# Kernel tuning notes

Measured on AMD Instinct MI355X. Metric: run time of the kernel, lower is better.

Reference implementation:

```python
import jax, jax.numpy as jnp
import numpy as np

HEADS = 16
D_MODEL = 1024
HEAD_DIM = D_MODEL // HEADS


def setup_inputs() -> dict:
    key = jax.random.key(0)
    ks = jax.random.split(key, 11)
    B, S, D = 2, 2048, D_MODEL
    s = 1.0 / np.sqrt(D)
    inp = {
        'Q': jax.random.normal(ks[0], (B, S, D), jnp.float32),
        'K': jax.random.normal(ks[1], (B, S, D), jnp.float32),
        'V': jax.random.normal(ks[2], (B, S, D), jnp.float32),
        'Wq': jax.random.normal(ks[3], (D, D), jnp.float32) * s,
        'Wk': jax.random.normal(ks[4], (D, D), jnp.float32) * s,
        'Wv': jax.random.normal(ks[5], (D, D), jnp.float32) * s,
        'Wo': jax.random.normal(ks[6], (D, D), jnp.float32) * s,
        'bq': jnp.zeros((D,), jnp.float32),
        'bk': jnp.zeros((D,), jnp.float32),
        'bv': jnp.zeros((D,), jnp.float32),
        'bo': jnp.zeros((D,), jnp.float32),
    }
    return inp


def reference(Q, K, V, Wq, Wk, Wv, Wo, bq, bk, bv, bo):
    B, S, D = Q.shape
    H, Dh = HEADS, HEAD_DIM
    # projections (torch Linear: x @ W.T + b)
    q = (Q @ Wq.T + bq).reshape(B, S, H, Dh).transpose(0, 2, 1, 3)  # [B,H,S,Dh]
    k = (K @ Wk.T + bk).reshape(B, S, H, Dh).transpose(0, 2, 1, 3)
    v = (V @ Wv.T + bv).reshape(B, S, H, Dh).transpose(0, 2, 1, 3)
    # naive scaled dot-product attention, scale = 1/sqrt(head_dim)
    scores = jnp.einsum('bhqd,bhkd->bhqk', q, k) / jnp.sqrt(jnp.float32(Dh))
    attn = jax.nn.softmax(scores, axis=-1)
    out = jnp.einsum('bhqk,bhkd->bhqd', attn, v)
    concat = out.transpose(0, 2, 1, 3).reshape(B, S, D)
    return concat @ Wo.T + bo
```

## Files before the change

kernel.cpp:

```cpp
#include <hip/hip_runtime.h>
#include <hip/hip_bf16.h>


#define SEQ     2048
#define DMODEL  1024
#define NHEADS  16
#define DH      64
#define MROWS   4096
#define M1      (1024*1024)
#define M4      (4*1024*1024)
#define SCQ     0.18033688f

typedef __hip_bfloat16 bf16;
typedef __attribute__((ext_vector_type(8))) short  short8;
typedef __attribute__((ext_vector_type(4))) float  f32x4;

__device__ __forceinline__ bf16 f2b(float x) { return __float2bfloat16(x); }
__device__ __forceinline__ f32x4 mfma16(short8 a, short8 b, f32x4 c) {
    return __builtin_amdgcn_mfma_f32_16x16x32_bf16(a, b, c, 0, 0, 0);
}
__device__ __forceinline__ unsigned pk2(float a, float b) {
    union { __hip_bfloat162 h; unsigned u; } x;
    x.h = __float22bfloat162_rn(float2{a, b});
    return x.u;
}
__device__ __forceinline__ short8 pk8(float4 a, float4 b) {
    union { short8 s; unsigned u[4]; } x;
    x.u[0] = pk2(a.x, a.y); x.u[1] = pk2(a.z, a.w);
    x.u[2] = pk2(b.x, b.y); x.u[3] = pk2(b.z, b.w);
    return x.s;
}
__device__ __forceinline__ float fexp2(float x) {
    return __builtin_amdgcn_exp2f(x);
}
#define GLDS(g, l) __builtin_amdgcn_global_load_lds( \
    (const __attribute__((address_space(1))) void*)(g), \
    (__attribute__((address_space(3))) void*)(l), 16, 0, 0)

__global__ __launch_bounds__(256) void cvt_all(
    const float* __restrict__ Wq, const float* __restrict__ Wk,
    const float* __restrict__ Wv, const float* __restrict__ Wo,
    const float* __restrict__ Q,  const float* __restrict__ K,
    const float* __restrict__ V,  bf16* __restrict__ dst)
{
    const size_t gid = (size_t)blockIdx.x * 256 + threadIdx.x;
    const size_t e0 = gid * 8;
    const float* s;
    if (e0 < (size_t)4 * M1) {
        const float* w[4] = {Wq, Wk, Wv, Wo};
        s = w[e0 >> 20] + (e0 & (M1 - 1));
    } else {
        const float* a[4] = {nullptr, Q, K, V};
        s = a[e0 >> 22] + (e0 & (M4 - 1));
    }
    float4 x = *(const float4*)s, y = *(const float4*)(s + 4);
    *(short8*)((short*)dst + e0) = pk8(x, y);
}

__global__ __launch_bounds__(256) void cvt_w(
    const float* __restrict__ W0, const float* __restrict__ W1,
    const float* __restrict__ W2, const float* __restrict__ W3,
    bf16* __restrict__ dst)
{
    const int gid = blockIdx.x * 256 + threadIdx.x;
    const int t   = gid >> 17;
    const int off = (gid & 131071) * 8;
    const float* srcs[4] = {W0, W1, W2, W3};
    const float* s = srcs[t] + off;
    float4 a = *(const float4*)s, b = *(const float4*)(s + 4);
    *(short8*)((short*)dst + (size_t)gid * 8) = pk8(a, b);
}

__global__ __launch_bounds__(256) void cvt_1(
    const float* __restrict__ X, bf16* __restrict__ D)
{
    const int gid = blockIdx.x * 256 + threadIdx.x;
    const int off = gid * 8;
    float4 a = *(const float4*)(X + off), b = *(const float4*)(X + off + 4);
    *(short8*)((short*)D + off) = pk8(a, b);
}

template <int BN>
__device__ __forceinline__ void gemm_body(
    const bf16* __restrict__ A, const bf16* __restrict__ B,
    const float* __restrict__ bias, void* __restrict__ outp,
    int m0, int n0, int mode, int bias_m, float scale)
{
    __shared__ short As[128 * 32];
    __shared__ short Bs[BN * 32];
    constexpr int NI = BN / 32;

    const int tid  = threadIdx.x;
    const int lane = tid & 63;
    const int wv   = tid >> 6;
    const int wm   = (wv >> 1) * 64;
    const int wn   = (wv & 1) * (BN / 2);
    const int fn   = lane & 15;
    const int fq   = lane >> 4;

    const int srow = lane >> 2;
    const int scol = (lane & 3) * 8;

    const short* Ag = (const short*)A;
    const short* Bg = (const short*)B;

    f32x4 acc[4][NI];
#pragma unroll
    for (int i = 0; i < 4; ++i)
#pragma unroll
        for (int j = 0; j < NI; ++j) acc[i][j] = (f32x4){0.f, 0.f, 0.f, 0.f};

    for (int k0 = 0; k0 < DMODEL; k0 += 32) {
#pragma unroll
        for (int i = 0; i < 2; ++i) {
            const int rr = wv * 32 + i * 16;
            const short* ga = Ag + (size_t)(m0 + rr + srow) * DMODEL + k0 + scol;
            GLDS(ga, As + rr * 32);
        }
#pragma unroll
        for (int i = 0; i < BN / 64; ++i) {
            const int rr = wv * (BN / 4) + i * 16;
            const short* gb = Bg + (size_t)(n0 + rr + srow) * DMODEL + k0 + scol;
            GLDS(gb, Bs + rr * 32);
        }
        __syncthreads();

        short8 af[4], bfr[NI];
#pragma unroll
        for (int im = 0; im < 4; ++im)
            af[im] = *(const short8*)(As + (wm + im * 16 + fn) * 32 + fq * 8);
#pragma unroll
        for (int in = 0; in < NI; ++in)
            bfr[in] = *(const short8*)(Bs + (wn + in * 16 + fn) * 32 + fq * 8);
#pragma unroll
        for (int im = 0; im < 4; ++im)
#pragma unroll
            for (int in = 0; in < NI; ++in)
                acc[im][in] = mfma16(af[im], bfr[in], acc[im][in]);
        __syncthreads();
    }

#pragma unroll
    for (int im = 0; im < 4; ++im) {
#pragma unroll
        for (int in = 0; in < NI; ++in) {
#pragma unroll
            for (int r = 0; r < 4; ++r) {
                const int m = m0 + wm + im * 16 + fq * 4 + r;
                const int n = n0 + wn + in * 16 + fn;
                const float c = (acc[im][in][r] + (bias_m ? bias[m] : bias[n])) * scale;
                if (mode == 0) {
                    ((float*)outp)[(size_t)m * DMODEL + n] = c;
                } else if (mode == 1) {
                    const int b = m >> 11, s = m & (SEQ - 1);
                    const int h = n >> 6,  d = n & (DH - 1);
                    ((bf16*)outp)[(((size_t)(b * NHEADS + h) * SEQ) + s) * DH + d] = f2b(c);
                } else {
                    const int h = m >> 6,  d = m & (DH - 1);
                    const int b = n >> 11, s = n & (SEQ - 1);
                    const int p = s & 31;
                    const int sp = (s & ~31) | ((p & 12) << 1) | ((p & 16) >> 2) | (p & 3);
                    ((bf16*)outp)[(((size_t)(b * NHEADS + h) * DH) + d) * SEQ + sp] = f2b(c);
                }
            }
        }
    }
}

__global__ __launch_bounds__(256, 3) void gemm_one(
    const bf16* A, const bf16* B, const float* bias, void* out,
    int mode, int bias_m, float scale)
{
    gemm_body<128>(A, B, bias, out, blockIdx.x * 128, blockIdx.y * 128,
                   mode, bias_m, scale);
}

__global__ __launch_bounds__(256, 3) void gemm_fin(
    const bf16* A, const bf16* B, const float* bias, void* out)
{
    gemm_body<64>(A, B, bias, out, blockIdx.x * 128, blockIdx.y * 64, 0, 0, 1.f);
}

__global__ __launch_bounds__(256, 3) void gemm_qkv(
    const bf16* Qb, const bf16* Kb, const bf16* Vb, const bf16* Wb,
    const float* bq, const float* bk, const float* bv,
    bf16* qp, bf16* kp, bf16* vp)
{
    const int blk = blockIdx.x;
    const int z = blk >> 8, t = blk & 255;
    if (z == 0)
        gemm_body<128>(Qb, Wb,          bq, qp, (t >> 3) * 128, (t & 7) * 128, 1, 0, SCQ);
    else if (z == 1)
        gemm_body<128>(Kb, Wb + M1,     bk, kp, (t >> 3) * 128, (t & 7) * 128, 1, 0, 1.f);
    else
        gemm_body<128>(Wb + 2 * M1, Vb, bv, vp, (t >> 5) * 128, (t & 31) * 128, 2, 1, 1.f);
}


#define QKG(KTB, G, S0, S1) { \
    const short* kr_ = (KTB) + ((G) * 16 + n) * 64; \
    short8 kf0_ = *(const short8*)(kr_ + off0); \
    short8 kf1_ = *(const short8*)(kr_ + off1); \
    S0 = mfma16(kf0_, qf00, Zv); S0 = mfma16(kf1_, qf01, S0); \
    S1 = mfma16(kf0_, qf10, Zv); S1 = mfma16(kf1_, qf11, S1); }

#define PKP(SA, SB, DST) { \
    union { short8 s8; unsigned u[4]; } bb_; \
    bb_.u[0] = pk2(fexp2(SA[0]), fexp2(SA[1])); \
    bb_.u[1] = pk2(fexp2(SA[2]), fexp2(SA[3])); \
    bb_.u[2] = pk2(fexp2(SB[0]), fexp2(SB[1])); \
    bb_.u[3] = pk2(fexp2(SB[2]), fexp2(SB[3])); \
    DST = bb_.s8; }

#define XPH(T, P00, P01, P10, P11) { \
    const short* KtB_ = Kb0 + ((T) & 1) * 4096; \
    f32x4 sa0_, sa1_, sb0_, sb1_; \
    QKG(KtB_, 0, sa0_, sa1_) \
    QKG(KtB_, 1, sb0_, sb1_) \
    PKP(sa0_, sb0_, P00) \
    PKP(sa1_, sb1_, P01) \
    QKG(KtB_, 2, sa0_, sa1_) \
    QKG(KtB_, 3, sb0_, sb1_) \
    PKP(sa0_, sb0_, P10) \
    PKP(sa1_, sb1_, P11) }

#define PVG(VTB, GD, P00, P01, P10, P11) { \
    const short* vr_ = (VTB) + ((GD) * 16 + n) * 64; \
    short8 vf0_ = *(const short8*)(vr_ + off0); \
    short8 vf1_ = *(const short8*)(vr_ + off1); \
    O[GD][0] = mfma16(vf0_, P00, O[GD][0]); \
    O[GD][0] = mfma16(vf1_, P10, O[GD][0]); \
    O[GD][1] = mfma16(vf0_, P01, O[GD][1]); \
    O[GD][1] = mfma16(vf1_, P11, O[GD][1]); }

#define YPH(T, P00, P01, P10, P11) { \
    const short* VtB_ = Vb0 + ((T) & 1) * 4096; \
    lc0 = mfma16(onesv, P00, lc0); \
    lc1 = mfma16(onesv, P01, lc1); \
    lc0 = mfma16(onesv, P10, lc0); \
    lc1 = mfma16(onesv, P11, lc1); \
    PVG(VtB_, 0, P00, P01, P10, P11) \
    PVG(VtB_, 1, P00, P01, P10, P11) \
    PVG(VtB_, 2, P00, P01, P10, P11) \
    PVG(VtB_, 3, P00, P01, P10, P11) }

__global__ __launch_bounds__(512, 4) void attn_fused(
    const bf16* __restrict__ q,
    const bf16* __restrict__ k,
    const bf16* __restrict__ vt,
    bf16* __restrict__ out)
{
    __shared__ short LB[32768];

    const int tid  = threadIdx.x;
    const int wave = tid >> 6;
    const int half = wave >> 2;
    const int w4   = wave & 3;
    const int lane = tid & 63;
    const int n    = lane & 15;
    const int quad = lane >> 4;

    const int blk  = blockIdx.x;
    const int xcd  = blk & 7;
    const int rest = blk >> 3;
    const int qt   = rest & 15;
    const int bh   = ((rest >> 4) << 3) | xcd;
    const int q0w  = qt * 128 + w4 * 32;
    const int kt0  = half * 16;

    const bf16* qhead = q  + (size_t)bh * SEQ * DH;
    const bf16* khead = k  + (size_t)bh * SEQ * DH;
    const bf16* vhead = vt + (size_t)bh * DH * SEQ;

    short* Kb0 = LB + half * 16384;
    short* Vb0 = LB + half * 16384 + 8192;

    short8 qf00, qf01, qf10, qf11;
    {
        const short* qr0 = (const short*)(qhead + (size_t)(q0w + n) * DH);
        qf00 = *(const short8*)(qr0 + quad * 8);
        qf01 = *(const short8*)(qr0 + 32 + quad * 8);
        const short* qr1 = (const short*)(qhead + (size_t)(q0w + 16 + n) * DH);
        qf10 = *(const short8*)(qr1 + quad * 8);
        qf11 = *(const short8*)(qr1 + 32 + quad * 8);
    }

    const short8 onesv = {(short)0x3F80, (short)0x3F80, (short)0x3F80, (short)0x3F80,
                          (short)0x3F80, (short)0x3F80, (short)0x3F80, (short)0x3F80};
    const f32x4 Zv = (f32x4){0.f, 0.f, 0.f, 0.f};

    f32x4 O[4][2];
#pragma unroll
    for (int gd = 0; gd < 4; ++gd)
#pragma unroll
        for (int qg = 0; qg < 2; ++qg) O[gd][qg] = Zv;
    f32x4 lc0 = Zv, lc1 = Zv;

    const int srow = lane >> 3;
    const int schk = (lane & 7) ^ srow;
    const int off0 = ((quad       ^ (n & 7)) * 8);
    const int off1 = (((4 + quad) ^ (n & 7)) * 8);

    auto stageK = [&](int kt, int buf) {
        const int kbase = kt * 64;
#pragma unroll
        for (int i = 0; i < 2; ++i) {
            const int r = w4 * 16 + i * 8 + srow;
            const char* gk = (const char*)(khead + (size_t)(kbase + r) * DH) + schk * 16;
            GLDS(gk, Kb0 + buf * 4096 + (w4 * 16 + i * 8) * 64);
        }
    };
    auto stageV = [&](int kt, int buf) {
        const int kbase = kt * 64;
#pragma unroll
        for (int i = 0; i < 2; ++i) {
            const int r = w4 * 16 + i * 8 + srow;
            const char* gv = (const char*)(vhead + (size_t)r * SEQ + kbase) + schk * 16;
            GLDS(gv, Vb0 + buf * 4096 + (w4 * 16 + i * 8) * 64);
        }
    };

    short8 PA00, PA01, PA10, PA11;
    short8 PB00, PB01, PB10, PB11;

    stageK(kt0, 0);

    __syncthreads();
    stageK(kt0 + 1, 1);
    stageV(kt0, 0);
    XPH(0, PA00, PA01, PA10, PA11)

#pragma unroll 1
    for (int t = 1; t < 15; t += 2) {
        __syncthreads();
        stageK(kt0 + t + 1, (t + 1) & 1);
        stageV(kt0 + t, t & 1);
        XPH(t, PB00, PB01, PB10, PB11)
        YPH(t - 1, PA00, PA01, PA10, PA11)
        __syncthreads();
        stageK(kt0 + t + 2, (t + 2) & 1);
        stageV(kt0 + t + 1, (t + 1) & 1);
        XPH(t + 1, PA00, PA01, PA10, PA11)
        YPH(t, PB00, PB01, PB10, PB11)
    }
    __syncthreads();
    stageV(kt0 + 15, 1);
    XPH(15, PB00, PB01, PB10, PB11)
    YPH(14, PA00, PA01, PA10, PA11)
    __syncthreads();
    YPH(15, PB00, PB01, PB10, PB11)

    float* scr = (float*)LB + (size_t)(w4 * 64 + lane) * 34;
    const float l0 = lc0[0];
    const float l1 = lc1[0];

    __syncthreads();
    if (half == 1) {
#pragma unroll
        for (int gd = 0; gd < 4; ++gd)
#pragma unroll
            for (int qg = 0; qg < 2; ++qg) {
                *(float2*)(scr + (gd * 2 + qg) * 4)     = float2{O[gd][qg][0], O[gd][qg][1]};
                *(float2*)(scr + (gd * 2 + qg) * 4 + 2) = float2{O[gd][qg][2], O[gd][qg][3]};
            }
        *(float2*)(scr + 32) = float2{l0, l1};
    }
    __syncthreads();
    if (half == 0) {
        const float2 lo = *(const float2*)(scr + 32);
        const float inv0 = 1.0f / (l0 + lo.x);
        const float inv1 = 1.0f / (l1 + lo.y);
        const int b = bh >> 4;
        const int h = bh & (NHEADS - 1);
#pragma unroll
        for (int gd = 0; gd < 4; ++gd) {
#pragma unroll
            for (int qg = 0; qg < 2; ++qg) {
                const float iv = qg ? inv1 : inv0;
                float2 a = *(const float2*)(scr + (gd * 2 + qg) * 4);
                float2 c = *(const float2*)(scr + (gd * 2 + qg) * 4 + 2);
                const int s = q0w + qg * 16 + n;
                uint2 o;
                o.x = pk2((O[gd][qg][0] + a.x) * iv, (O[gd][qg][1] + a.y) * iv);
                o.y = pk2((O[gd][qg][2] + c.x) * iv, (O[gd][qg][3] + c.y) * iv);
                *(uint2*)(out + ((size_t)(b * SEQ + s)) * DMODEL + h * DH + gd * 16 + quad * 4) = o;
            }
        }
    }
}

#undef QKG
#undef PKP
#undef XPH
#undef PVG
#undef YPH

__global__ __launch_bounds__(256) void attn_mfma(
    const bf16* __restrict__ q,
    const bf16* __restrict__ k,
    const bf16* __restrict__ vt,
    bf16* __restrict__ out)
{
    __shared__ short Kt[2][64 * 64];
    __shared__ short Vt[2][64 * 64];

    const int tid  = threadIdx.x;
    const int wave = tid >> 6;
    const int lane = tid & 63;
    const int n    = lane & 15;
    const int quad = lane >> 4;

    const int blk  = blockIdx.x;
    const int xcd  = blk & 7;
    const int rest = blk >> 3;
    const int qt   = rest & 15;
    const int bh   = ((rest >> 4) << 3) | xcd;
    const int q0w  = qt * 128 + wave * 32;

    const bf16* qhead = q  + (size_t)bh * SEQ * DH;
    const bf16* khead = k  + (size_t)bh * SEQ * DH;
    const bf16* vhead = vt + (size_t)bh * DH * SEQ;

    short8 qf[2][2];
#pragma unroll
    for (int qg = 0; qg < 2; ++qg) {
        const short* qr = (const short*)(qhead + (size_t)(q0w + qg * 16 + n) * DH);
        qf[qg][0] = *(const short8*)(qr + quad * 8);
        qf[qg][1] = *(const short8*)(qr + 32 + quad * 8);
    }

    const short8 onesv = {(short)0x3F80, (short)0x3F80, (short)0x3F80, (short)0x3F80,
                          (short)0x3F80, (short)0x3F80, (short)0x3F80, (short)0x3F80};
    const f32x4 Zv = (f32x4){0.f, 0.f, 0.f, 0.f};

    f32x4 O[4][2];
#pragma unroll
    for (int gd = 0; gd < 4; ++gd)
#pragma unroll
        for (int qg = 0; qg < 2; ++qg) O[gd][qg] = Zv;
    f32x4 lacc[2] = {Zv, Zv};

    const int srow = lane >> 3;
    const int schk = (lane & 7) ^ srow;
    const int off0 = ((quad       ^ (n & 7)) * 8);
    const int off1 = (((4 + quad) ^ (n & 7)) * 8);

    auto stage = [&](int kt, int buf) {
        const int kbase = kt * 64;
#pragma unroll
        for (int i = 0; i < 2; ++i) {
            const int r = wave * 16 + i * 8 + srow;
            const char* gk = (const char*)(khead + (size_t)(kbase + r) * DH) + schk * 16;
            const char* gv = (const char*)(vhead + (size_t)r * SEQ + kbase) + schk * 16;
            GLDS(gk, Kt[buf] + (wave * 16 + i * 8) * 64);
            GLDS(gv, Vt[buf] + (wave * 16 + i * 8) * 64);
        }
    };

    auto tile_body = [&](const short* KtB, const short* VtB) {
        f32x4 st[4][2];
#pragma unroll
        for (int g = 0; g < 4; ++g) {
            const short* kr = KtB + (g * 16 + n) * 64;
            short8 kf0 = *(const short8*)(kr + off0);
            short8 kf1 = *(const short8*)(kr + off1);
#pragma unroll
            for (int qg = 0; qg < 2; ++qg) {
                f32x4 s = mfma16(kf0, qf[qg][0], Zv);
                s = mfma16(kf1, qf[qg][1], s);
                st[g][qg] = s;
            }
        }
        short8 bP[2][2];
#pragma unroll
        for (int t = 0; t < 2; ++t) {
#pragma unroll
            for (int qg = 0; qg < 2; ++qg) {
                union { short8 s8; unsigned u[4]; } bb;
                bb.u[0] = pk2(fexp2(st[2*t][qg][0]),   fexp2(st[2*t][qg][1]));
                bb.u[1] = pk2(fexp2(st[2*t][qg][2]),   fexp2(st[2*t][qg][3]));
                bb.u[2] = pk2(fexp2(st[2*t+1][qg][0]), fexp2(st[2*t+1][qg][1]));
                bb.u[3] = pk2(fexp2(st[2*t+1][qg][2]), fexp2(st[2*t+1][qg][3]));
                bP[t][qg] = bb.s8;
                lacc[qg] = mfma16(onesv, bP[t][qg], lacc[qg]);
            }
        }
#pragma unroll
        for (int gd = 0; gd < 4; ++gd) {
            const short* vr = VtB + (gd * 16 + n) * 64;
            short8 vf0 = *(const short8*)(vr + off0);
            short8 vf1 = *(const short8*)(vr + off1);
#pragma unroll
            for (int qg = 0; qg < 2; ++qg) {
                O[gd][qg] = mfma16(vf0, bP[0][qg], O[gd][qg]);
                O[gd][qg] = mfma16(vf1, bP[1][qg], O[gd][qg]);
            }
        }
    };

    stage(0, 0);
#pragma unroll 1
    for (int kt = 0; kt < SEQ / 64; kt += 2) {
        __syncthreads();
        stage(kt + 1, 1);
        tile_body(Kt[0], Vt[0]);
        __syncthreads();
        if (kt + 2 < SEQ / 64) stage(kt + 2, 0);
        tile_body(Kt[1], Vt[1]);
    }

    const float inv0 = 1.0f / lacc[0][0];
    const float inv1 = 1.0f / lacc[1][0];
    const int b = bh >> 4;
    const int h = bh & (NHEADS - 1);
#pragma unroll
    for (int gd = 0; gd < 4; ++gd) {
#pragma unroll
        for (int qg = 0; qg < 2; ++qg) {
            const float iv = qg ? inv1 : inv0;
            const int s = q0w + qg * 16 + n;
            uint2 o;
            o.x = pk2(O[gd][qg][0] * iv, O[gd][qg][1] * iv);
            o.y = pk2(O[gd][qg][2] * iv, O[gd][qg][3] * iv);
            *(uint2*)(out + ((size_t)(b * SEQ + s)) * DMODEL + h * DH + gd * 16 + quad * 4) = o;
        }
    }
}

extern "C" void kernel_launch(void* const* d_in, const int* in_sizes, int n_in,
                              void* d_out, int out_size, void* d_ws, size_t ws_size,
                              hipStream_t stream) {
    const float* Q  = (const float*)d_in[0];
    const float* K  = (const float*)d_in[1];
    const float* V  = (const float*)d_in[2];
    const float* Wq = (const float*)d_in[3];
    const float* Wk = (const float*)d_in[4];
    const float* Wv = (const float*)d_in[5];
    const float* Wo = (const float*)d_in[6];
    const float* bq = (const float*)d_in[7];
    const float* bk = (const float*)d_in[8];
    const float* bv = (const float*)d_in[9];
    const float* bo = (const float*)d_in[10];

    bf16* kp = (bf16*)d_out;
    bf16* vp = kp + M4;

    dim3 bb(256);
    dim3 gqk(MROWS / 128, DMODEL / 128);
    dim3 gvv(DMODEL / 128, MROWS / 128);
    dim3 gfin(MROWS / 128, DMODEL / 64);

    if (ws_size >= (size_t)40 * 1024 * 1024) {
        bf16* Wb = (bf16*)d_ws;
        bf16* Qb = Wb + 4 * M1;
        bf16* Kb = Qb + M4;
        bf16* Vb = Kb + M4;
        bf16* qp = Vb + M4;
        bf16* ao = Qb;

        cvt_all<<<8192, bb, 0, stream>>>(Wq, Wk, Wv, Wo, Q, K, V, Wb);
        gemm_qkv<<<768, bb, 0, stream>>>(Qb, Kb, Vb, Wb, bq, bk, bv, qp, kp, vp);
        attn_fused<<<512, 512, 0, stream>>>(qp, kp, vp, ao);
        gemm_fin<<<gfin, bb, 0, stream>>>(ao, Wb + 3 * M1, bo, d_out);
    } else {
        bf16* Wb = (bf16*)d_ws;
        bf16* Xb = Wb + 4 * M1;
        bf16* qp = Xb + M4;
        bf16* ao = Xb;

        cvt_w<<<2048, bb, 0, stream>>>(Wq, Wk, Wv, Wo, Wb);
        cvt_1<<<2048, bb, 0, stream>>>(Q, Xb);
        gemm_one<<<gqk, bb, 0, stream>>>(Xb, Wb, bq, qp, 1, 0, SCQ);
        cvt_1<<<2048, bb, 0, stream>>>(K, Xb);
        gemm_one<<<gqk, bb, 0, stream>>>(Xb, Wb + M1, bk, kp, 1, 0, 1.f);
        cvt_1<<<2048, bb, 0, stream>>>(V, Xb);
        gemm_one<<<gvv, bb, 0, stream>>>(Wb + 2 * M1, Xb, bv, vp, 2, 1, 1.f);
        attn_mfma<<<512, bb, 0, stream>>>(qp, kp, vp, ao);
        gemm_fin<<<gfin, bb, 0, stream>>>(ao, Wb + 3 * M1, bo, d_out);
    }
}
```

Measured before the change: 209.9 us.

## Give each attention wave 64 query rows with 256-thread blocks

Blocks in the fused attention kernel drop from 8 waves to 4, so each wave now handles 64 query rows instead of 32. Every K and V fragment read from shared memory then feeds twice as many MFMAs, and staging is split across fewer waves with more loads each. The cost is roughly doubled accumulator and P registers per wave, plus fewer waves per block to hide latency.

```diff
diff --git a/kernel.cpp b/kernel.cpp
--- a/kernel.cpp
+++ b/kernel.cpp
@@ -197,54 +197,53 @@
 }
 
 
-#define QKG(KTB, G, S0, S1) { \
-    const short* kr_ = (KTB) + ((G) * 16 + n) * 64; \
-    short8 kf0_ = *(const short8*)(kr_ + off0); \
-    short8 kf1_ = *(const short8*)(kr_ + off1); \
-    S0 = mfma16(kf0_, qf00, Zv); S0 = mfma16(kf1_, qf01, S0); \
-    S1 = mfma16(kf0_, qf10, Zv); S1 = mfma16(kf1_, qf11, S1); }
-
-#define PKP(SA, SB, DST) { \
-    union { short8 s8; unsigned u[4]; } bb_; \
-    bb_.u[0] = pk2(fexp2(SA[0]), fexp2(SA[1])); \
-    bb_.u[1] = pk2(fexp2(SA[2]), fexp2(SA[3])); \
-    bb_.u[2] = pk2(fexp2(SB[0]), fexp2(SB[1])); \
-    bb_.u[3] = pk2(fexp2(SB[2]), fexp2(SB[3])); \
-    DST = bb_.s8; }
-
-#define XPH(T, P00, P01, P10, P11) { \
+#define XPH(T, P) { \
     const short* KtB_ = Kb0 + ((T) & 1) * 4096; \
-    f32x4 sa0_, sa1_, sb0_, sb1_; \
-    QKG(KtB_, 0, sa0_, sa1_) \
-    QKG(KtB_, 1, sb0_, sb1_) \
-    PKP(sa0_, sb0_, P00) \
-    PKP(sa1_, sb1_, P01) \
-    QKG(KtB_, 2, sa0_, sa1_) \
-    QKG(KtB_, 3, sb0_, sb1_) \
-    PKP(sa0_, sb0_, P10) \
-    PKP(sa1_, sb1_, P11) }
-
-#define PVG(VTB, GD, P00, P01, P10, P11) { \
-    const short* vr_ = (VTB) + ((GD) * 16 + n) * 64; \
-    short8 vf0_ = *(const short8*)(vr_ + off0); \
-    short8 vf1_ = *(const short8*)(vr_ + off1); \
-    O[GD][0] = mfma16(vf0_, P00, O[GD][0]); \
-    O[GD][0] = mfma16(vf1_, P10, O[GD][0]); \
-    O[GD][1] = mfma16(vf0_, P01, O[GD][1]); \
-    O[GD][1] = mfma16(vf1_, P11, O[GD][1]); }
-
-#define YPH(T, P00, P01, P10, P11) { \
+    _Pragma("unroll") \
+    for (int tt = 0; tt < 2; ++tt) { \
+        f32x4 st[2][4]; \
+        _Pragma("unroll") \
+        for (int g2 = 0; g2 < 2; ++g2) { \
+            const short* kr_ = KtB_ + ((tt * 2 + g2) * 16 + n) * 64; \
+            short8 kf0_ = *(const short8*)(kr_ + off0); \
+            short8 kf1_ = *(const short8*)(kr_ + off1); \
+            _Pragma("unroll") \
+            for (int qg = 0; qg < 4; ++qg) { \
+                f32x4 s_ = mfma16(kf0_, qf[qg][0], Zv); \
+                st[g2][qg] = mfma16(kf1_, qf[qg][1], s_); \
+            } \
+        } \
+        _Pragma("unroll") \
+        for (int qg = 0; qg < 4; ++qg) { \
+            union { short8 s8; unsigned u[4]; } bb_; \
+            bb_.u[0] = pk2(fexp2(st[0][qg][0]), fexp2(st[0][qg][1])); \
+            bb_.u[1] = pk2(fexp2(st[0][qg][2]), fexp2(st[0][qg][3])); \
+            bb_.u[2] = pk2(fexp2(st[1][qg][0]), fexp2(st[1][qg][1])); \
+            bb_.u[3] = pk2(fexp2(st[1][qg][2]), fexp2(st[1][qg][3])); \
+            P[tt][qg] = bb_.s8; \
+        } \
+    } }
+
+#define YPH(T, P) { \
     const short* VtB_ = Vb0 + ((T) & 1) * 4096; \
-    lc0 = mfma16(onesv, P00, lc0); \
-    lc1 = mfma16(onesv, P01, lc1); \
-    lc0 = mfma16(onesv, P10, lc0); \
-    lc1 = mfma16(onesv, P11, lc1); \
-    PVG(VtB_, 0, P00, P01, P10, P11) \
-    PVG(VtB_, 1, P00, P01, P10, P11) \
-    PVG(VtB_, 2, P00, P01, P10, P11) \
-    PVG(VtB_, 3, P00, P01, P10, P11) }
-
-__global__ __launch_bounds__(512, 4) void attn_fused(
+    _Pragma("unroll") \
+    for (int qg = 0; qg < 4; ++qg) { \
+        lc[qg] = mfma16(onesv, P[0][qg], lc[qg]); \
+        lc[qg] = mfma16(onesv, P[1][qg], lc[qg]); \
+    } \
+    _Pragma("unroll") \
+    for (int gd = 0; gd < 4; ++gd) { \
+        const short* vr_ = VtB_ + (gd * 16 + n) * 64; \
+        short8 vf0_ = *(const short8*)(vr_ + off0); \
+        short8 vf1_ = *(const short8*)(vr_ + off1); \
+        _Pragma("unroll") \
+        for (int qg = 0; qg < 4; ++qg) { \
+            O[gd][qg] = mfma16(vf0_, P[0][qg], O[gd][qg]); \
+            O[gd][qg] = mfma16(vf1_, P[1][qg], O[gd][qg]); \
+        } \
+    } }
+
+__global__ __launch_bounds__(256, 2) void attn_fused(
     const bf16* __restrict__ q,
     const bf16* __restrict__ k,
     const bf16* __restrict__ vt,
@@ -254,8 +253,8 @@
 
     const int tid  = threadIdx.x;
     const int wave = tid >> 6;
-    const int half = wave >> 2;
-    const int w4   = wave & 3;
+    const int half = wave >> 1;
+    const int wq   = wave & 1;
     const int lane = tid & 63;
     const int n    = lane & 15;
     const int quad = lane >> 4;
@@ -265,7 +264,7 @@
     const int rest = blk >> 3;
     const int qt   = rest & 15;
     const int bh   = ((rest >> 4) << 3) | xcd;
-    const int q0w  = qt * 128 + w4 * 32;
+    const int q0w  = qt * 128 + wq * 64;
     const int kt0  = half * 16;
 
     const bf16* qhead = q  + (size_t)bh * SEQ * DH;
@@ -275,26 +274,26 @@
     short* Kb0 = LB + half * 16384;
     short* Vb0 = LB + half * 16384 + 8192;
 
-    short8 qf00, qf01, qf10, qf11;
-    {
-        const short* qr0 = (const short*)(qhead + (size_t)(q0w + n) * DH);
-        qf00 = *(const short8*)(qr0 + quad * 8);
-        qf01 = *(const short8*)(qr0 + 32 + quad * 8);
-        const short* qr1 = (const short*)(qhead + (size_t)(q0w + 16 + n) * DH);
-        qf10 = *(const short8*)(qr1 + quad * 8);
-        qf11 = *(const short8*)(qr1 + 32 + quad * 8);
+    short8 qf[4][2];
+#pragma unroll
+    for (int qg = 0; qg < 4; ++qg) {
+        const short* qr = (const short*)(qhead + (size_t)(q0w + qg * 16 + n) * DH);
+        qf[qg][0] = *(const short8*)(qr + quad * 8);
+        qf[qg][1] = *(const short8*)(qr + 32 + quad * 8);
     }
 
     const short8 onesv = {(short)0x3F80, (short)0x3F80, (short)0x3F80, (short)0x3F80,
                           (short)0x3F80, (short)0x3F80, (short)0x3F80, (short)0x3F80};
     const f32x4 Zv = (f32x4){0.f, 0.f, 0.f, 0.f};
 
-    f32x4 O[4][2];
+    f32x4 O[4][4];
 #pragma unroll
     for (int gd = 0; gd < 4; ++gd)
 #pragma unroll
-        for (int qg = 0; qg < 2; ++qg) O[gd][qg] = Zv;
-    f32x4 lc0 = Zv, lc1 = Zv;
+        for (int qg = 0; qg < 4; ++qg) O[gd][qg] = Zv;
+    f32x4 lc[4];
+#pragma unroll
+    for (int qg = 0; qg < 4; ++qg) lc[qg] = Zv;
 
     const int srow = lane >> 3;
     const int schk = (lane & 7) ^ srow;
@@ -304,81 +303,81 @@
     auto stageK = [&](int kt, int buf) {
         const int kbase = kt * 64;
 #pragma unroll
-        for (int i = 0; i < 2; ++i) {
-            const int r = w4 * 16 + i * 8 + srow;
+        for (int i = 0; i < 4; ++i) {
+            const int r = wq * 32 + i * 8 + srow;
             const char* gk = (const char*)(khead + (size_t)(kbase + r) * DH) + schk * 16;
-            GLDS(gk, Kb0 + buf * 4096 + (w4 * 16 + i * 8) * 64);
+            GLDS(gk, Kb0 + buf * 4096 + (wq * 32 + i * 8) * 64);
         }
     };
     auto stageV = [&](int kt, int buf) {
         const int kbase = kt * 64;
 #pragma unroll
-        for (int i = 0; i < 2; ++i) {
-            const int r = w4 * 16 + i * 8 + srow;
+        for (int i = 0; i < 4; ++i) {
+            const int r = wq * 32 + i * 8 + srow;
             const char* gv = (const char*)(vhead + (size_t)r * SEQ + kbase) + schk * 16;
-            GLDS(gv, Vb0 + buf * 4096 + (w4 * 16 + i * 8) * 64);
+            GLDS(gv, Vb0 + buf * 4096 + (wq * 32 + i * 8) * 64);
         }
     };
 
-    short8 PA00, PA01, PA10, PA11;
-    short8 PB00, PB01, PB10, PB11;
+    short8 PA[2][4], PB[2][4];
 
     stageK(kt0, 0);
 
     __syncthreads();
     stageK(kt0 + 1, 1);
     stageV(kt0, 0);
-    XPH(0, PA00, PA01, PA10, PA11)
+    XPH(0, PA)
 
 #pragma unroll 1
     for (int t = 1; t < 15; t += 2) {
         __syncthreads();
         stageK(kt0 + t + 1, (t + 1) & 1);
         stageV(kt0 + t, t & 1);
-        XPH(t, PB00, PB01, PB10, PB11)
-        YPH(t - 1, PA00, PA01, PA10, PA11)
+        XPH(t, PB)
+        YPH(t - 1, PA)
         __syncthreads();
         stageK(kt0 + t + 2, (t + 2) & 1);
         stageV(kt0 + t + 1, (t + 1) & 1);
-        XPH(t + 1, PA00, PA01, PA10, PA11)
-        YPH(t, PB00, PB01, PB10, PB11)
+        XPH(t + 1, PA)
+        YPH(t, PB)
     }
     __syncthreads();
     stageV(kt0 + 15, 1);
-    XPH(15, PB00, PB01, PB10, PB11)
-    YPH(14, PA00, PA01, PA10, PA11)
+    XPH(15, PB)
+    YPH(14, PA)
     __syncthreads();
-    YPH(15, PB00, PB01, PB10, PB11)
-
-    float* scr = (float*)LB + (size_t)(w4 * 64 + lane) * 34;
-    const float l0 = lc0[0];
-    const float l1 = lc1[0];
+    YPH(15, PB)
+
+    float* scr = (float*)LB + (size_t)(wq * 64 + lane) * 68;
 
     __syncthreads();
     if (half == 1) {
 #pragma unroll
         for (int gd = 0; gd < 4; ++gd)
 #pragma unroll
-            for (int qg = 0; qg < 2; ++qg) {
-                *(float2*)(scr + (gd * 2 + qg) * 4)     = float2{O[gd][qg][0], O[gd][qg][1]};
-                *(float2*)(scr + (gd * 2 + qg) * 4 + 2) = float2{O[gd][qg][2], O[gd][qg][3]};
+            for (int qg = 0; qg < 4; ++qg) {
+                *(float2*)(scr + (gd * 4 + qg) * 4)     = float2{O[gd][qg][0], O[gd][qg][1]};
+                *(float2*)(scr + (gd * 4 + qg) * 4 + 2) = float2{O[gd][qg][2], O[gd][qg][3]};
             }
-        *(float2*)(scr + 32) = float2{l0, l1};
+        *(float4*)(scr + 64) = float4{lc[0][0], lc[1][0], lc[2][0], lc[3][0]};
     }
     __syncthreads();
     if (half == 0) {
-        const float2 lo = *(const float2*)(scr + 32);
-        const float inv0 = 1.0f / (l0 + lo.x);
-        const float inv1 = 1.0f / (l1 + lo.y);
+        const float4 lo = *(const float4*)(scr + 64);
+        float inv[4];
+        inv[0] = 1.0f / (lc[0][0] + lo.x);
+        inv[1] = 1.0f / (lc[1][0] + lo.y);
+        inv[2] = 1.0f / (lc[2][0] + lo.z);
+        inv[3] = 1.0f / (lc[3][0] + lo.w);
         const int b = bh >> 4;
         const int h = bh & (NHEADS - 1);
 #pragma unroll
         for (int gd = 0; gd < 4; ++gd) {
 #pragma unroll
-            for (int qg = 0; qg < 2; ++qg) {
-                const float iv = qg ? inv1 : inv0;
-                float2 a = *(const float2*)(scr + (gd * 2 + qg) * 4);
-                float2 c = *(const float2*)(scr + (gd * 2 + qg) * 4 + 2);
+            for (int qg = 0; qg < 4; ++qg) {
+                const float iv = inv[qg];
+                float2 a = *(const float2*)(scr + (gd * 4 + qg) * 4);
+                float2 c = *(const float2*)(scr + (gd * 4 + qg) * 4 + 2);
                 const int s = q0w + qg * 16 + n;
                 uint2 o;
                 o.x = pk2((O[gd][qg][0] + a.x) * iv, (O[gd][qg][1] + a.y) * iv);
@@ -389,10 +388,7 @@
     }
 }
 
-#undef QKG
-#undef PKP
 #undef XPH
-#undef PVG
 #undef YPH
 
 __global__ __launch_bounds__(256) void attn_mfma(
@@ -560,7 +556,7 @@
 
         cvt_all<<<8192, bb, 0, stream>>>(Wq, Wk, Wv, Wo, Q, K, V, Wb);
         gemm_qkv<<<768, bb, 0, stream>>>(Qb, Kb, Vb, Wb, bq, bk, bv, qp, kp, vp);
-        attn_fused<<<512, 512, 0, stream>>>(qp, kp, vp, ao);
+        attn_fused<<<512, 256, 0, stream>>>(qp, kp, vp, ao);
         gemm_fin<<<gfin, bb, 0, stream>>>(ao, Wb + 3 * M1, bo, d_out);
     } else {
         bf16* Wb = (bf16*)d_ws;
```

Result: no change. 212.7 us (+1.3%).
